# Kernel optimization log

Hardware: AMD Instinct MI355X
Metric: run time of the kernel (lower is better)

Reference implementation:

```python
import jax, jax.numpy as jnp
import numpy as np

NUM_CLASS = 80
S = 76              # output_size = 608 // 8 (scale i=0)
STRIDE = 8.0
XYSCALE = 1.2
IOU_LOSS_THRESH = 0.5
INPUT_SIZE = 608.0  # stride * output_size
ANCHORS0 = np.array([[12., 16.], [19., 36.], [40., 28.]], dtype=np.float32)


def setup_inputs() -> dict:
    key = jax.random.key(0)
    k1, k2, k3 = jax.random.split(key, 3)
    B, MAXGT = 16, 150
    conv = jax.random.normal(k1, (B, S, S, 3 * (5 + NUM_CLASS)), dtype=jnp.float32)
    label = jax.random.uniform(k2, (B, S, S, 3, 5 + NUM_CLASS), dtype=jnp.float32)
    # scale the xywh channels of label to pixel coordinates
    label = label.at[..., :4].multiply(INPUT_SIZE)
    bboxes = jax.random.uniform(k3, (B, MAXGT, 4), dtype=jnp.float32) * INPUT_SIZE
    return {"conv": conv, "label": label, "bboxes": bboxes}


def _bce_with_logits(logits, labels):
    # tf.nn.sigmoid_cross_entropy_with_logits, numerically stable form
    return jnp.maximum(logits, 0.0) - logits * labels + jnp.log1p(jnp.exp(-jnp.abs(logits)))


def _xywh_to_corners(b):
    return jnp.concatenate([b[..., :2] - b[..., 2:] * 0.5,
                            b[..., :2] + b[..., 2:] * 0.5], axis=-1)


def _bbox_iou(boxes1, boxes2):
    area1 = boxes1[..., 2] * boxes1[..., 3]
    area2 = boxes2[..., 2] * boxes2[..., 3]
    b1, b2 = _xywh_to_corners(boxes1), _xywh_to_corners(boxes2)
    lu = jnp.maximum(b1[..., :2], b2[..., :2])
    rd = jnp.minimum(b1[..., 2:], b2[..., 2:])
    inter = jnp.maximum(rd - lu, 0.0)
    inter_area = inter[..., 0] * inter[..., 1]
    union = area1 + area2 - inter_area
    return inter_area / union


def _bbox_giou(boxes1, boxes2):
    area1 = boxes1[..., 2] * boxes1[..., 3]
    area2 = boxes2[..., 2] * boxes2[..., 3]
    b1, b2 = _xywh_to_corners(boxes1), _xywh_to_corners(boxes2)
    lu = jnp.maximum(b1[..., :2], b2[..., :2])
    rd = jnp.minimum(b1[..., 2:], b2[..., 2:])
    inter = jnp.maximum(rd - lu, 0.0)
    inter_area = inter[..., 0] * inter[..., 1]
    union = area1 + area2 - inter_area
    iou = inter_area / union
    enc_lu = jnp.minimum(b1[..., :2], b2[..., :2])
    enc_rd = jnp.maximum(b1[..., 2:], b2[..., 2:])
    enc = jnp.maximum(enc_rd - enc_lu, 0.0)
    enc_area = enc[..., 0] * enc[..., 1]
    return iou - (enc_area - union) / enc_area


def _decode_train(conv):
    B = conv.shape[0]
    conv = conv.reshape(B, S, S, 3, 5 + NUM_CLASS)
    dxdy, dwdh, raw_conf, raw_prob = jnp.split(conv, [2, 4, 5], axis=-1)
    xs, ys = jnp.meshgrid(jnp.arange(S), jnp.arange(S))  # indexing='xy' like tf.meshgrid
    grid = jnp.stack([xs, ys], axis=-1)[None, :, :, None, :].astype(jnp.float32)  # [1,S,S,1,2]
    pred_xy = (jax.nn.sigmoid(dxdy) * XYSCALE - 0.5 * (XYSCALE - 1.0) + grid) * STRIDE
    pred_wh = jnp.exp(dwdh) * ANCHORS0  # [B,S,S,3,2]
    return jnp.concatenate([pred_xy, pred_wh,
                            jax.nn.sigmoid(raw_conf), jax.nn.sigmoid(raw_prob)], axis=-1)


def reference(conv, label, bboxes):
    pred = _decode_train(conv)  # [B,S,S,3,5+C]
    B = conv.shape[0]
    conv5 = conv.reshape(B, S, S, 3, 5 + NUM_CLASS)
    conv_raw_conf = conv5[..., 4:5]
    conv_raw_prob = conv5[..., 5:]

    pred_xywh = pred[..., 0:4]
    pred_conf = pred[..., 4:5]

    label_xywh = label[..., 0:4]
    respond_bbox = label[..., 4:5]
    label_prob = label[..., 5:]

    giou = _bbox_giou(pred_xywh, label_xywh)[..., None]
    bbox_loss_scale = 2.0 - label_xywh[..., 2:3] * label_xywh[..., 3:4] / (INPUT_SIZE ** 2)
    giou_loss = respond_bbox * bbox_loss_scale * (1.0 - giou)

    # pairwise IoU: [B,S,S,3,1,4] vs [B,1,1,1,MAXGT,4] -> [B,S,S,3,MAXGT]
    iou = _bbox_iou(pred_xywh[..., None, :], bboxes[:, None, None, None, :, :])
    max_iou = jnp.max(iou, axis=-1, keepdims=True)
    respond_bgd = (1.0 - respond_bbox) * (max_iou < IOU_LOSS_THRESH).astype(jnp.float32)

    conf_focal = jnp.square(respond_bbox - pred_conf)
    bce_conf = _bce_with_logits(conv_raw_conf, respond_bbox)
    conf_loss = conf_focal * (respond_bbox * bce_conf + respond_bgd * bce_conf)
    prob_loss = respond_bbox * _bce_with_logits(conv_raw_prob, label_prob)

    giou_loss = jnp.mean(jnp.sum(giou_loss, axis=(1, 2, 3, 4)))
    conf_loss = jnp.mean(jnp.sum(conf_loss, axis=(1, 2, 3, 4)))
    prob_loss = jnp.mean(jnp.sum(prob_loss, axis=(1, 2, 3, 4)))
    return jnp.stack([giou_loss, conf_loss, prob_loss])
```

## Files before the change

### kernel.cpp

```cpp
#include <hip/hip_runtime.h>
#include <math.h>

#define S 76
#define A 3
#define CH 85
#define NCLS 80
#define MAXGT 150
#define CPB (S * S * A)
#define FPB (CPB * CH)
#define BATCH 16
#define TOTF4 ((BATCH * FPB) / 4)
#define BLK 256
#define ROUNDS 8
#define STREAM_BLOCKS ((TOTF4 + BLK * ROUNDS - 1) / (BLK * ROUNDS))
#define ATILE 128
#define AGX ((CPB + ATILE - 1) / ATILE)
#define GEO_BLOCKS (AGX * BATCH)
#define TOT_BLOCKS (STREAM_BLOCKS + GEO_BLOCKS)

__device__ __forceinline__ float frcp(float x) { return __builtin_amdgcn_rcpf(x); }
__device__ __forceinline__ float sigmoidf_(float x) { return frcp(1.f + __expf(-x)); }
__device__ __forceinline__ float bcef(float x, float y) {
    const float t  = __builtin_amdgcn_exp2f(x * 1.44269504f);
    const float lg = __builtin_amdgcn_logf(1.f + t);
    return __builtin_fmaf(0.69314718f, lg, -x * y);
}

__global__ __launch_bounds__(BLK, 1) void yolo_fused_kernel(
    const float* __restrict__ conv, const float* __restrict__ label,
    const float* __restrict__ bboxes, float* __restrict__ partA ,
    float* __restrict__ partB )
{
    const unsigned bid = blockIdx.x;
    const int tid = threadIdx.x;
    const unsigned geo_before = (unsigned)(((unsigned long long)bid * GEO_BLOCKS) / TOT_BLOCKS);
    const unsigned geo_after  = (unsigned)(((unsigned long long)(bid + 1) * GEO_BLOCKS) / TOT_BLOCKS);

    if (geo_after == geo_before) {
        const unsigned sidx = bid - geo_before;
        const int base = (int)sidx * (BLK * ROUNDS);
        const float4* __restrict__ cv4 = (const float4*)conv;
        const float4* __restrict__ lb4 = (const float4*)label;

        float p_sum = 0.f;

        if (sidx + 1 < STREAM_BLOCKS) {
            float4 c_s[ROUNDS], l_s[ROUNDS];
            float  rs_s[ROUNDS];
            unsigned r0_s[ROUNDS];
            #pragma unroll
            for (int r = 0; r < ROUNDS; ++r) {
                const int u = base + r * BLK + tid;
                c_s[r] = cv4[(size_t)u];
                l_s[r] = lb4[(size_t)u];
                const unsigned e0 = 4u * (unsigned)u;
                const unsigned c0 = e0 / 85u;
                r0_s[r] = e0 - 85u * c0;
                rs_s[r] = label[(size_t)c0 * CH + 4];
            }
            __builtin_amdgcn_sched_barrier(0);
            #pragma unroll
            for (int r = 0; r < ROUNDS; ++r) {
                const float4 cc = c_s[r];
                const float4 lc = l_s[r];
                const float rspc = rs_s[r];
                const unsigned r0c = r0_s[r];
                const float cx[4] = {cc.x, cc.y, cc.z, cc.w};
                const float lx[4] = {lc.x, lc.y, lc.z, lc.w};
                float s = 0.f;
                #pragma unroll
                for (int k = 0; k < 4; ++k) {
                    const unsigned rr = r0c + k;
                    const float bv = bcef(cx[k], lx[k]);
                    s += ((rr - 5u) < 80u) ? bv : 0.f;
                }
                p_sum = __builtin_fmaf(rspc, s, p_sum);
            }
        } else {
            for (int r = 0; r < ROUNDS; ++r) {
                const int u = base + r * BLK + tid;
                if (u >= TOTF4) break;
                const float4 cc = cv4[(size_t)u];
                const float4 lc = lb4[(size_t)u];
                const unsigned e0 = 4u * (unsigned)u;
                const unsigned c0 = e0 / 85u;
                const unsigned r0c = e0 - 85u * c0;
                const float rspc = label[(size_t)c0 * CH + 4];
                const float cx[4] = {cc.x, cc.y, cc.z, cc.w};
                const float lx[4] = {lc.x, lc.y, lc.z, lc.w};
                float s = 0.f;
                #pragma unroll
                for (int k = 0; k < 4; ++k) {
                    const unsigned rr = r0c + k;
                    const float bv = bcef(cx[k], lx[k]);
                    s += ((rr - 5u) < 80u) ? bv : 0.f;
                }
                p_sum = __builtin_fmaf(rspc, s, p_sum);
            }
        }

        for (int off = 32; off > 0; off >>= 1) p_sum += __shfl_down(p_sum, off, 64);
        __shared__ float sredp[BLK / 64];
        const int lane = tid & 63, wv = tid >> 6;
        if (lane == 0) sredp[wv] = p_sum;
        __syncthreads();
        if (tid == 0) {
            float P = 0.f;
            #pragma unroll
            for (int w = 0; w < BLK / 64; ++w) P += sredp[w];
            partB[sidx] = P;
        }
    } else {
        const unsigned gidx = geo_before;
        const int b    = gidx / AGX;
        const int tile = gidx - b * AGX;

        __shared__ float4 s_box[MAXGT];
        __shared__ float  s_ba[MAXGT];

        const int ci = tid >> 1;
        const int pr = tid & 1;
        const int t = tile * ATILE + ci;
        const bool valid = (t < CPB);
        const int tc = valid ? t : (CPB - 1);

        const size_t boff = (size_t)b * FPB;
        const float* cv = conv  + boff + (size_t)tc * CH;
        const float* lb = label + boff + (size_t)tc * CH;

        if (tid < MAXGT) {
            const float4 bx = *(const float4*)(bboxes + (size_t)b * (MAXGT * 4) + tid * 4);
            const float hw = bx.z * 0.5f, hh = bx.w * 0.5f;
            s_box[tid] = make_float4(3.f * (bx.x - hw), bx.y - hh, 3.f * (bx.x + hw), bx.y + hh);
            s_ba[tid]  = bx.z * bx.w;
        }
        const float dx = cv[0], dy = cv[1], dw = cv[2], dh = cv[3], rc = cv[4];
        const float lx = lb[0], ly = lb[1], lw = lb[2], lh = lb[3], resp = lb[4];
        __syncthreads();

        const int i   = tc / (S * A);
        const int rem = tc - i * (S * A);
        const int j   = rem / A;
        const int a   = rem - j * A;
        const float aw = (a == 0) ? 12.f : ((a == 1) ? 19.f : 40.f);
        const float ah = (a == 0) ? 16.f : ((a == 1) ? 36.f : 28.f);

        const float px = (sigmoidf_(dx) * 1.2f - 0.1f + (float)j) * 8.f;
        const float py = (sigmoidf_(dy) * 1.2f - 0.1f + (float)i) * 8.f;
        const float pw = __expf(dw) * aw;
        const float ph = __expf(dh) * ah;
        const float pconf = sigmoidf_(rc);

        const float px1 = px - pw * 0.5f, py1 = py - ph * 0.5f;
        const float px2 = px + pw * 0.5f, py2 = py + ph * 0.5f;
        const float areap = pw * ph;

        const float px1_3 = 3.f * px1, px2_3 = 3.f * px2;
        float maxv = -1e30f;
        #pragma unroll 5
        for (int k = pr; k < MAXGT; k += 2) {
            const float4 bx = s_box[k];
            const float ba  = s_ba[k];
            const float kiw3 = fmaxf(fminf(px2_3, bx.z) - fmaxf(px1_3, bx.x), 0.f);
            const float kih  = fmaxf(fminf(py2, bx.w) - fmaxf(py1, bx.y), 0.f);
            maxv = fmaxf(maxv, __builtin_fmaf(kiw3, kih, -ba));
        }
        maxv = fmaxf(maxv, __shfl_xor(maxv, 1, 64));

        float g_sum = 0.f, c_sum = 0.f;
        if (pr == 0 && valid) {
            const float lx1 = lx - lw * 0.5f, ly1 = ly - lh * 0.5f;
            const float lx2 = lx + lw * 0.5f, ly2 = ly + lh * 0.5f;
            const float areal = lw * lh;
            const float iw = fmaxf(fminf(px2, lx2) - fmaxf(px1, lx1), 0.f);
            const float ih = fmaxf(fminf(py2, ly2) - fmaxf(py1, ly1), 0.f);
            const float inter = iw * ih;
            const float uni = areap + areal - inter;
            const float iou = inter * frcp(uni);
            const float ew = fmaxf(fmaxf(px2, lx2) - fminf(px1, lx1), 0.f);
            const float eh = fmaxf(fmaxf(py2, ly2) - fminf(py1, ly1), 0.f);
            const float enc = ew * eh;
            const float giou = iou - (enc - uni) * frcp(enc);
            g_sum = resp * (2.f - areal * (1.f / (608.f * 608.f))) * (1.f - giou);

            const float bgd = (1.f - resp) * ((maxv < areap) ? 1.f : 0.f);
            const float focal = (resp - pconf) * (resp - pconf);
            c_sum = focal * (resp + bgd) * bcef(rc, resp);
        }

        for (int off = 32; off > 0; off >>= 1) {
            g_sum += __shfl_down(g_sum, off, 64);
            c_sum += __shfl_down(c_sum, off, 64);
        }
        __shared__ float sred[2][BLK / 64];
        const int lane = tid & 63, wv = tid >> 6;
        if (lane == 0) { sred[0][wv] = g_sum; sred[1][wv] = c_sum; }
        __syncthreads();
        if (tid == 0) {
            float G = 0.f, C = 0.f;
            #pragma unroll
            for (int w = 0; w < BLK / 64; ++w) { G += sred[0][w]; C += sred[1][w]; }
            partA[gidx * 2 + 0] = G;
            partA[gidx * 2 + 1] = C;
        }
    }
}

__global__ __launch_bounds__(256) void final_reduce(
    const float* __restrict__ partA, const float* __restrict__ partB,
    float* __restrict__ out, int nA, int nB, float invB)
{
    const int tid = threadIdx.x;
    float g = 0.f, c = 0.f, p = 0.f;
    for (int k = tid; k < nA; k += 256) { g += partA[2 * k]; c += partA[2 * k + 1]; }
    for (int k = tid; k < nB; k += 256) p += partB[k];
    for (int off = 32; off > 0; off >>= 1) {
        g += __shfl_down(g, off, 64);
        c += __shfl_down(c, off, 64);
        p += __shfl_down(p, off, 64);
    }
    __shared__ float sred[3][4];
    const int lane = tid & 63, wv = tid >> 6;
    if (lane == 0) { sred[0][wv] = g; sred[1][wv] = c; sred[2][wv] = p; }
    __syncthreads();
    if (tid == 0) {
        float G = 0.f, C = 0.f, P = 0.f;
        #pragma unroll
        for (int w = 0; w < 4; ++w) { G += sred[0][w]; C += sred[1][w]; P += sred[2][w]; }
        out[0] = G * invB;
        out[1] = C * invB;
        out[2] = P * invB;
    }
}

extern "C" void kernel_launch(void* const* d_in, const int* in_sizes, int n_in,
                              void* d_out, int out_size, void* d_ws, size_t ws_size,
                              hipStream_t stream) {
    const float* conv   = (const float*)d_in[0];
    const float* label  = (const float*)d_in[1];
    const float* bboxes = (const float*)d_in[2];
    float* out  = (float*)d_out;
    float* wsf  = (float*)d_ws;
    float* partA = wsf;
    float* partB = wsf + 8192;

    yolo_fused_kernel<<<TOT_BLOCKS, BLK, 0, stream>>>(conv, label, bboxes, partA, partB);
    final_reduce<<<1, 256, 0, stream>>>(partA, partB, out, GEO_BLOCKS, STREAM_BLOCKS,
                                        1.f / (float)BATCH);
}
```

Before: 59.38 us.

## Software-pipeline stream loads with inline asm waits and LDS-staged respond values

```diff
diff --git a/kernel.cpp b/kernel.cpp
--- a/kernel.cpp
+++ b/kernel.cpp
@@ -4,7 +4,6 @@
 #define S 76
 #define A 3
 #define CH 85
-#define NCLS 80
 #define MAXGT 150
 #define CPB (S * S * A)
 #define FPB (CPB * CH)
@@ -12,11 +11,15 @@
 #define TOTF4 ((BATCH * FPB) / 4)
 #define BLK 256
 #define ROUNDS 8
+#define DEPTH 4
 #define STREAM_BLOCKS ((TOTF4 + BLK * ROUNDS - 1) / (BLK * ROUNDS))
 #define ATILE 128
 #define AGX ((CPB + ATILE - 1) / ATILE)
 #define GEO_BLOCKS (AGX * BATCH)
 #define TOT_BLOCKS (STREAM_BLOCKS + GEO_BLOCKS)
+#define MAXC 392
+
+typedef float fx4 __attribute__((ext_vector_type(4)));
 
 __device__ __forceinline__ float frcp(float x) { return __builtin_amdgcn_rcpf(x); }
 __device__ __forceinline__ float sigmoidf_(float x) { return frcp(1.f + __expf(-x)); }
@@ -26,11 +29,26 @@
     return __builtin_fmaf(0.69314718f, lg, -x * y);
 }
 
-__global__ __launch_bounds__(BLK, 1) void yolo_fused_kernel(
+template<int N>
+__device__ __forceinline__ void vmwait() {
+    asm volatile("s_waitcnt vmcnt(%0)" :: "i"(N));
+    __builtin_amdgcn_sched_barrier(0);
+}
+__device__ __forceinline__ void gload4(fx4& d, const float* p) {
+    asm volatile("global_load_dwordx4 %0, %1, off" : "=v"(d) : "v"(p));
+}
+
+__global__ __launch_bounds__(BLK, 6) void yolo_fused_kernel(
     const float* __restrict__ conv, const float* __restrict__ label,
     const float* __restrict__ bboxes, float* __restrict__ partA ,
     float* __restrict__ partB )
 {
+    __shared__ float  s_resp[MAXC];
+    __shared__ float  sredp[BLK / 64];
+    __shared__ float4 s_box[MAXGT];
+    __shared__ float  s_ba[MAXGT];
+    __shared__ float  sred2[2][BLK / 64];
+
     const unsigned bid = blockIdx.x;
     const int tid = threadIdx.x;
     const unsigned geo_before = (unsigned)(((unsigned long long)bid * GEO_BLOCKS) / TOT_BLOCKS);
@@ -39,44 +57,55 @@
     if (geo_after == geo_before) {
         const unsigned sidx = bid - geo_before;
         const int base = (int)sidx * (BLK * ROUNDS);
-        const float4* __restrict__ cv4 = (const float4*)conv;
-        const float4* __restrict__ lb4 = (const float4*)label;
-
         float p_sum = 0.f;
 
         if (sidx + 1 < STREAM_BLOCKS) {
-            float4 c_s[ROUNDS], l_s[ROUNDS];
-            float  rs_s[ROUNDS];
-            unsigned r0_s[ROUNDS];
+            const unsigned base_e = 4u * (unsigned)base;
+            const unsigned cstart = base_e / 85u;
+            const unsigned cend   = (base_e + BLK * ROUNDS * 4u - 1u) / 85u;
+            const int nc = (int)(cend - cstart) + 1;
+            for (int i = tid; i < nc; i += BLK)
+                s_resp[i] = label[(size_t)(cstart + i) * CH + 4];
+            __syncthreads();
+
+            const float* pc0 = conv  + ((size_t)base + (size_t)tid) * 4;
+            const float* pl0 = label + ((size_t)base + (size_t)tid) * 4;
+            fx4 c_s[DEPTH], l_s[DEPTH];
             #pragma unroll
-            for (int r = 0; r < ROUNDS; ++r) {
-                const int u = base + r * BLK + tid;
-                c_s[r] = cv4[(size_t)u];
-                l_s[r] = lb4[(size_t)u];
-                const unsigned e0 = 4u * (unsigned)u;
-                const unsigned c0 = e0 / 85u;
-                r0_s[r] = e0 - 85u * c0;
-                rs_s[r] = label[(size_t)c0 * CH + 4];
+            for (int s = 0; s < DEPTH; ++s) {
+                gload4(c_s[s], pc0 + s * (BLK * 4));
+                gload4(l_s[s], pl0 + s * (BLK * 4));
             }
-            __builtin_amdgcn_sched_barrier(0);
-            #pragma unroll
-            for (int r = 0; r < ROUNDS; ++r) {
-                const float4 cc = c_s[r];
-                const float4 lc = l_s[r];
-                const float rspc = rs_s[r];
-                const unsigned r0c = r0_s[r];
-                const float cx[4] = {cc.x, cc.y, cc.z, cc.w};
-                const float lx[4] = {lc.x, lc.y, lc.z, lc.w};
-                float s = 0.f;
-                #pragma unroll
-                for (int k = 0; k < 4; ++k) {
-                    const unsigned rr = r0c + k;
-                    const float bv = bcef(cx[k], lx[k]);
-                    s += ((rr - 5u) < 80u) ? bv : 0.f;
-                }
-                p_sum = __builtin_fmaf(rspc, s, p_sum);
+            #define STEP(R, W)                                                      \
+            {                                                                       \
+                vmwait<W>();                                                        \
+                const fx4 cc = c_s[(R) & 3];                                        \
+                const fx4 lc = l_s[(R) & 3];                                        \
+                const unsigned e0 = 4u * (unsigned)(base + (R) * BLK + tid);        \
+                const unsigned c0 = e0 / 85u;                                       \
+                const unsigned r0 = e0 - 85u * c0;                                  \
+                const float rsp = s_resp[c0 - cstart];                              \
+                const float cxx[4] = {cc.x, cc.y, cc.z, cc.w};                      \
+                const float lxx[4] = {lc.x, lc.y, lc.z, lc.w};                      \
+                float s_ = 0.f;                                                     \
+                _Pragma("unroll")                                                   \
+                for (int k = 0; k < 4; ++k) {                                       \
+                    const unsigned rr = r0 + (unsigned)k;                           \
+                    const float bv = bcef(cxx[k], lxx[k]);                          \
+                    s_ += ((rr - 5u) < 80u) ? bv : 0.f;                             \
+                }                                                                   \
+                p_sum = __builtin_fmaf(rsp, s_, p_sum);                             \
+                if ((R) + DEPTH < ROUNDS) {                                         \
+                    gload4(c_s[(R) & 3], pc0 + ((R) + DEPTH) * (BLK * 4));          \
+                    gload4(l_s[(R) & 3], pl0 + ((R) + DEPTH) * (BLK * 4));          \
+                }                                                                   \
             }
+            STEP(0, 6) STEP(1, 6) STEP(2, 6) STEP(3, 6)
+            STEP(4, 6) STEP(5, 4) STEP(6, 2) STEP(7, 0)
+            #undef STEP
         } else {
+            const float4* cv4 = (const float4*)conv;
+            const float4* lb4 = (const float4*)label;
             for (int r = 0; r < ROUNDS; ++r) {
                 const int u = base + r * BLK + tid;
                 if (u >= TOTF4) break;
@@ -86,21 +115,20 @@
                 const unsigned c0 = e0 / 85u;
                 const unsigned r0c = e0 - 85u * c0;
                 const float rspc = label[(size_t)c0 * CH + 4];
-                const float cx[4] = {cc.x, cc.y, cc.z, cc.w};
-                const float lx[4] = {lc.x, lc.y, lc.z, lc.w};
-                float s = 0.f;
+                const float cxx[4] = {cc.x, cc.y, cc.z, cc.w};
+                const float lxx[4] = {lc.x, lc.y, lc.z, lc.w};
+                float s_ = 0.f;
                 #pragma unroll
                 for (int k = 0; k < 4; ++k) {
                     const unsigned rr = r0c + k;
-                    const float bv = bcef(cx[k], lx[k]);
-                    s += ((rr - 5u) < 80u) ? bv : 0.f;
+                    const float bv = bcef(cxx[k], lxx[k]);
+                    s_ += ((rr - 5u) < 80u) ? bv : 0.f;
                 }
-                p_sum = __builtin_fmaf(rspc, s, p_sum);
+                p_sum = __builtin_fmaf(rspc, s_, p_sum);
             }
         }
 
         for (int off = 32; off > 0; off >>= 1) p_sum += __shfl_down(p_sum, off, 64);
-        __shared__ float sredp[BLK / 64];
         const int lane = tid & 63, wv = tid >> 6;
         if (lane == 0) sredp[wv] = p_sum;
         __syncthreads();
@@ -114,9 +142,6 @@
         const unsigned gidx = geo_before;
         const int b    = gidx / AGX;
         const int tile = gidx - b * AGX;
-
-        __shared__ float4 s_box[MAXGT];
-        __shared__ float  s_ba[MAXGT];
 
         const int ci = tid >> 1;
         const int pr = tid & 1;
@@ -192,14 +217,13 @@
             g_sum += __shfl_down(g_sum, off, 64);
             c_sum += __shfl_down(c_sum, off, 64);
         }
-        __shared__ float sred[2][BLK / 64];
         const int lane = tid & 63, wv = tid >> 6;
-        if (lane == 0) { sred[0][wv] = g_sum; sred[1][wv] = c_sum; }
+        if (lane == 0) { sred2[0][wv] = g_sum; sred2[1][wv] = c_sum; }
         __syncthreads();
         if (tid == 0) {
             float G = 0.f, C = 0.f;
             #pragma unroll
-            for (int w = 0; w < BLK / 64; ++w) { G += sred[0][w]; C += sred[1][w]; }
+            for (int w = 0; w < BLK / 64; ++w) { G += sred2[0][w]; C += sred2[1][w]; }
             partA[gidx * 2 + 0] = G;
             partA[gidx * 2 + 1] = C;
         }
```

Result: slower. 64.03 us (+7.8%).
